# Kernel optimization log

Measured on AMD Instinct MI355X. Metric: run time of the kernel, lower is better.

The kernel has to match this reference:

```python
import jax, jax.numpy as jnp
import numpy as np

N, IN_DIM, OUT_DIM, HEADS = 3072, 512, 64, 8
EDGE_PROB = 0.01
NEG_SLOPE = 0.2


def setup_inputs() -> dict:
    key = jax.random.key(0)
    k1, k2, k3, k4, k5 = jax.random.split(key, 5)
    x = jax.random.normal(k1, (N, IN_DIM), dtype=jnp.float32)
    # sparse-ish dense adjacency mask with self-loops
    adj = (jax.random.uniform(k2, (N, N)) < EDGE_PROB).astype(jnp.float32)
    adj = jnp.maximum(adj, jnp.eye(N, dtype=jnp.float32))
    W = jax.random.normal(k3, (HEADS, IN_DIM, OUT_DIM), dtype=jnp.float32) * 0.1
    a_src = jax.random.normal(k4, (HEADS, OUT_DIM), dtype=jnp.float32) * 0.1
    a_dst = jax.random.normal(k5, (HEADS, OUT_DIM), dtype=jnp.float32) * 0.1
    return {"x": x, "adj": adj, "W": W, "a_src": a_src, "a_dst": a_dst}


def reference(x, adj, W, a_src, a_dst):
    # per-head linear projection: [H, N, OUT]
    h = jnp.einsum("ni,hio->hno", x, W)
    # attention logits e_ij = LeakyReLU(a_src . h_i + a_dst . h_j)
    f_src = jnp.einsum("hno,ho->hn", h, a_src)  # [H, N]
    f_dst = jnp.einsum("hno,ho->hn", h, a_dst)  # [H, N]
    e = f_src[:, :, None] + f_dst[:, None, :]   # [H, N, N]
    e = jax.nn.leaky_relu(e, negative_slope=NEG_SLOPE)
    # mask non-edges, row-softmax over neighbors
    e = jnp.where(adj[None] > 0, e, jnp.float32(-1e9))
    att = jax.nn.softmax(e, axis=-1)             # [H, N, N]
    # aggregate neighbor features per head
    out = jnp.einsum("hij,hjo->hio", att, h)     # [H, N, OUT]
    # concat heads along feature dim -> [N, H*OUT]
    return out.transpose(1, 0, 2).reshape(N, HEADS * OUT_DIM)
```

## Files before the change

kernel.cpp:

```cpp
#include <hip/hip_runtime.h>

#define N_NODES 3072
#define IN_DIM 512
#define OUT_DIM 64
#define HEADS 8
#define NEG_SLOPE 0.2f
#define MAX_E 128
#define KTILES (IN_DIM / 32)

typedef __attribute__((ext_vector_type(8))) short bf16x8;
typedef __attribute__((ext_vector_type(4))) float f32x4;

__device__ inline unsigned short f2bf(float f) {
    union { float f; unsigned u; } v; v.f = f;
    unsigned r = (v.u + 0x7FFF + ((v.u >> 16) & 1)) >> 16;
    return (unsigned short)r;
}

__global__ __launch_bounds__(256, 3) void gat_proj(
    const float* __restrict__ x, const float* __restrict__ W,
    const float* __restrict__ a_src, const float* __restrict__ a_dst,
    unsigned short* __restrict__ hb, float* __restrict__ fsrc,
    float* __restrict__ fdst) {
    __shared__ float hs[32][OUT_DIM + 1];

    const int t = threadIdx.x;
    const int lane = t & 63;
    const int w = t >> 6;
    const int head = blockIdx.y;
    const int m0 = blockIdx.x * 32;

    const int colr = lane & 15;
    const int kq = lane >> 4;

    const float* wp0 = W + ((size_t)head * IN_DIM + kq * 8) * OUT_DIM + w * 16 + colr;
    const float* xr0 = x + (size_t)(m0 + colr) * IN_DIM + kq * 8;
    const float* xr1 = xr0 + (size_t)16 * IN_DIM;

    f32x4 acc0 = {0.f, 0.f, 0.f, 0.f};
    f32x4 acc1 = {0.f, 0.f, 0.f, 0.f};
#pragma unroll
    for (int kt = 0; kt < KTILES; ++kt) {
        const float* wp = wp0 + (size_t)kt * 32 * OUT_DIM;
        bf16x8 bv;
#pragma unroll
        for (int j = 0; j < 8; ++j) bv[j] = (short)f2bf(wp[(size_t)j * OUT_DIM]);

        const float4* p0 = (const float4*)(xr0 + kt * 32);
        const float4* p1 = (const float4*)(xr1 + kt * 32);
        float4 u0 = p0[0], u1 = p0[1];
        float4 v0 = p1[0], v1 = p1[1];
        bf16x8 a0, a1;
        a0[0] = (short)f2bf(u0.x); a0[1] = (short)f2bf(u0.y);
        a0[2] = (short)f2bf(u0.z); a0[3] = (short)f2bf(u0.w);
        a0[4] = (short)f2bf(u1.x); a0[5] = (short)f2bf(u1.y);
        a0[6] = (short)f2bf(u1.z); a0[7] = (short)f2bf(u1.w);
        a1[0] = (short)f2bf(v0.x); a1[1] = (short)f2bf(v0.y);
        a1[2] = (short)f2bf(v0.z); a1[3] = (short)f2bf(v0.w);
        a1[4] = (short)f2bf(v1.x); a1[5] = (short)f2bf(v1.y);
        a1[6] = (short)f2bf(v1.z); a1[7] = (short)f2bf(v1.w);
        acc0 = __builtin_amdgcn_mfma_f32_16x16x32_bf16(a0, bv, acc0, 0, 0, 0);
        acc1 = __builtin_amdgcn_mfma_f32_16x16x32_bf16(a1, bv, acc1, 0, 0, 0);
    }

    const int col = w * 16 + colr;
    const int r0 = kq * 4;
    unsigned short* hp = hb + (size_t)m0 * (HEADS * OUT_DIM) + head * OUT_DIM + col;
#pragma unroll
    for (int i2 = 0; i2 < 4; ++i2) {
        hs[r0 + i2][col] = acc0[i2];
        hs[r0 + 16 + i2][col] = acc1[i2];
        hp[(size_t)(r0 + i2) * (HEADS * OUT_DIM)] = f2bf(acc0[i2]);
        hp[(size_t)(r0 + 16 + i2) * (HEADS * OUT_DIM)] = f2bf(acc1[i2]);
    }
    __syncthreads();

    {
        const float* av = (t < 128 ? a_src : a_dst) + head * OUT_DIM;
        const int tt = t & 127;
        const int row = tt >> 2, part = tt & 3;
        float s = 0.f;
#pragma unroll
        for (int n = 0; n < 16; ++n) s += hs[row][part * 16 + n] * av[part * 16 + n];
        s += __shfl_xor(s, 1, 64);
        s += __shfl_xor(s, 2, 64);
        if (part == 0) {
            float* dst = (t < 128 ? fsrc : fdst);
            dst[head * N_NODES + m0 + row] = s;
        }
    }
}

__global__ __launch_bounds__(256) void gat_agg(
    const float* __restrict__ adj, const unsigned short* __restrict__ hb,
    const float* __restrict__ fsrc, const float* __restrict__ fdst,
    float* __restrict__ out) {
    __shared__ int s_idx[MAX_E];
    __shared__ float s_p[HEADS][MAX_E];
    __shared__ int s_cnt;

    const int i = blockIdx.x;
    const int t = threadIdx.x;
    if (t == 0) s_cnt = 0;
    __syncthreads();

    const float4* arow4 = (const float4*)(adj + (size_t)i * N_NODES);
#pragma unroll
    for (int it = 0; it < 3; ++it) {
        const int jj = t + it * 256;
        float4 v = arow4[jj];
        const int j = jj * 4;
        if (v.x > 0.f) { int s = atomicAdd(&s_cnt, 1); if (s < MAX_E) s_idx[s] = j; }
        if (v.y > 0.f) { int s = atomicAdd(&s_cnt, 1); if (s < MAX_E) s_idx[s] = j + 1; }
        if (v.z > 0.f) { int s = atomicAdd(&s_cnt, 1); if (s < MAX_E) s_idx[s] = j + 2; }
        if (v.w > 0.f) { int s = atomicAdd(&s_cnt, 1); if (s < MAX_E) s_idx[s] = j + 3; }
    }
    __syncthreads();
    const int E = min(s_cnt, MAX_E);

    const int w = t >> 6;
    const int lane = t & 63;
    const int half = lane >> 5;
    const int sl = lane & 31;
    const int head = 2 * w + half;

    const float fi = fsrc[head * N_NODES + i];

    float m = -1e30f;
    for (int k = sl; k < E; k += 32) {
        float e = fi + fdst[head * N_NODES + s_idx[k]];
        e = e > 0.f ? e : NEG_SLOPE * e;
        s_p[head][k] = e;
        m = fmaxf(m, e);
    }
#pragma unroll
    for (int o = 16; o; o >>= 1) m = fmaxf(m, __shfl_xor(m, o, 64));

    float sum = 0.f;
    for (int k = sl; k < E; k += 32) {
        float p = __expf(s_p[head][k] - m);
        s_p[head][k] = p;
        sum += p;
    }
#pragma unroll
    for (int o = 16; o; o >>= 1) sum += __shfl_xor(sum, o, 64);
    const float inv = 1.f / sum;

    __syncthreads();

    const unsigned short* hbase = hb + head * OUT_DIM + sl * 2;
    float a0 = 0.f, a1 = 0.f;
#pragma unroll 8
    for (int k = 0; k < E; ++k) {
        const int j = s_idx[k];
        const float p = s_p[head][k];
        const unsigned u = *(const unsigned*)(hbase + (size_t)j * (HEADS * OUT_DIM));
        a0 = fmaf(p, __uint_as_float(u << 16), a0);
        a1 = fmaf(p, __uint_as_float(u & 0xffff0000u), a1);
    }
    float2 r = {a0 * inv, a1 * inv};
    *(float2*)(out + (size_t)i * (HEADS * OUT_DIM) + head * OUT_DIM + sl * 2) = r;
}

extern "C" void kernel_launch(void* const* d_in, const int* in_sizes, int n_in,
                              void* d_out, int out_size, void* d_ws, size_t ws_size,
                              hipStream_t stream) {
    const float* x     = (const float*)d_in[0];
    const float* adj   = (const float*)d_in[1];
    const float* W     = (const float*)d_in[2];
    const float* a_src = (const float*)d_in[3];
    const float* a_dst = (const float*)d_in[4];
    float* out = (float*)d_out;

    float* fsrc = (float*)d_ws;
    float* fdst = fsrc + HEADS * N_NODES;
    unsigned short* hb = (unsigned short*)(fdst + HEADS * N_NODES);

    gat_proj<<<dim3(N_NODES / 32, HEADS), 256, 0, stream>>>(
        x, W, a_src, a_dst, hb, fsrc, fdst);
    gat_agg<<<N_NODES, 256, 0, stream>>>(adj, hb, fsrc, fdst, out);
}
```

Baseline: 124.1 us.

## Move adjacency scan into projection kernel and stage x tile in LDS

Appends adjacency-row scan blocks to the projection launch so the memory-bound adj scan runs alongside the projection MFMA work. The scan writes neighbor indices and counts to workspace, and the aggregation kernel then only reads the compacted list. The projection now converts the x tile to bf16 once into swizzled shared memory instead of reading it per k-tile from global. The cost is extra workspace traffic for the index lists and a heterogeneous grid with 32KB shared memory per block.

New measurement: 107.3 us. 13.5% less time.

```diff
diff --git a/kernel.cpp b/kernel.cpp
--- a/kernel.cpp
+++ b/kernel.cpp
@@ -7,6 +7,7 @@
 #define NEG_SLOPE 0.2f
 #define MAX_E 128
 #define KTILES (IN_DIM / 32)
+#define PROJ_BLOCKS (N_NODES / 32 * HEADS)
 
 typedef __attribute__((ext_vector_type(8))) short bf16x8;
 typedef __attribute__((ext_vector_type(4))) float f32x4;
@@ -17,65 +18,79 @@
     return (unsigned short)r;
 }
 
-__global__ __launch_bounds__(256, 3) void gat_proj(
+__global__ __launch_bounds__(256) void gat_proj_scan(
     const float* __restrict__ x, const float* __restrict__ W,
+    const float* __restrict__ adj,
     const float* __restrict__ a_src, const float* __restrict__ a_dst,
     unsigned short* __restrict__ hb, float* __restrict__ fsrc,
-    float* __restrict__ fdst) {
-    __shared__ float hs[32][OUT_DIM + 1];
-
+    float* __restrict__ fdst, int* __restrict__ e_idx, int* __restrict__ e_cnt) {
+    __shared__ __align__(16) char smem[32768];
+
+    const int b = blockIdx.x;
     const int t = threadIdx.x;
-    const int lane = t & 63;
-    const int w = t >> 6;
-    const int head = blockIdx.y;
-    const int m0 = blockIdx.x * 32;
-
-    const int colr = lane & 15;
-    const int kq = lane >> 4;
-
-    const float* wp0 = W + ((size_t)head * IN_DIM + kq * 8) * OUT_DIM + w * 16 + colr;
-    const float* xr0 = x + (size_t)(m0 + colr) * IN_DIM + kq * 8;
-    const float* xr1 = xr0 + (size_t)16 * IN_DIM;
-
-    f32x4 acc0 = {0.f, 0.f, 0.f, 0.f};
-    f32x4 acc1 = {0.f, 0.f, 0.f, 0.f};
-#pragma unroll
-    for (int kt = 0; kt < KTILES; ++kt) {
-        const float* wp = wp0 + (size_t)kt * 32 * OUT_DIM;
-        bf16x8 bv;
-#pragma unroll
-        for (int j = 0; j < 8; ++j) bv[j] = (short)f2bf(wp[(size_t)j * OUT_DIM]);
-
-        const float4* p0 = (const float4*)(xr0 + kt * 32);
-        const float4* p1 = (const float4*)(xr1 + kt * 32);
-        float4 u0 = p0[0], u1 = p0[1];
-        float4 v0 = p1[0], v1 = p1[1];
-        bf16x8 a0, a1;
-        a0[0] = (short)f2bf(u0.x); a0[1] = (short)f2bf(u0.y);
-        a0[2] = (short)f2bf(u0.z); a0[3] = (short)f2bf(u0.w);
-        a0[4] = (short)f2bf(u1.x); a0[5] = (short)f2bf(u1.y);
-        a0[6] = (short)f2bf(u1.z); a0[7] = (short)f2bf(u1.w);
-        a1[0] = (short)f2bf(v0.x); a1[1] = (short)f2bf(v0.y);
-        a1[2] = (short)f2bf(v0.z); a1[3] = (short)f2bf(v0.w);
-        a1[4] = (short)f2bf(v1.x); a1[5] = (short)f2bf(v1.y);
-        a1[6] = (short)f2bf(v1.z); a1[7] = (short)f2bf(v1.w);
-        acc0 = __builtin_amdgcn_mfma_f32_16x16x32_bf16(a0, bv, acc0, 0, 0, 0);
-        acc1 = __builtin_amdgcn_mfma_f32_16x16x32_bf16(a1, bv, acc1, 0, 0, 0);
-    }
-
-    const int col = w * 16 + colr;
-    const int r0 = kq * 4;
-    unsigned short* hp = hb + (size_t)m0 * (HEADS * OUT_DIM) + head * OUT_DIM + col;
-#pragma unroll
-    for (int i2 = 0; i2 < 4; ++i2) {
-        hs[r0 + i2][col] = acc0[i2];
-        hs[r0 + 16 + i2][col] = acc1[i2];
-        hp[(size_t)(r0 + i2) * (HEADS * OUT_DIM)] = f2bf(acc0[i2]);
-        hp[(size_t)(r0 + 16 + i2) * (HEADS * OUT_DIM)] = f2bf(acc1[i2]);
-    }
-    __syncthreads();
-
-    {
+
+    if (b < PROJ_BLOCKS) {
+        short* xs = (short*)smem;
+        const int lane = t & 63;
+        const int w = t >> 6;
+        const int head = b / 96;
+        const int rtp = b % 96;
+        const int m0 = rtp * 32;
+
+        {
+            const int r = t >> 3, c8 = t & 7;
+            const float* xrow = x + (size_t)(m0 + r) * IN_DIM;
+#pragma unroll
+            for (int qq = 0; qq < 8; ++qq) {
+                const int k0 = c8 * 8 + qq * 64;
+                const float4* xp = (const float4*)(xrow + k0);
+                float4 v0 = xp[0], v1 = xp[1];
+                bf16x8 rv;
+                rv[0] = (short)f2bf(v0.x); rv[1] = (short)f2bf(v0.y);
+                rv[2] = (short)f2bf(v0.z); rv[3] = (short)f2bf(v0.w);
+                rv[4] = (short)f2bf(v1.x); rv[5] = (short)f2bf(v1.y);
+                rv[6] = (short)f2bf(v1.z); rv[7] = (short)f2bf(v1.w);
+                const int kt = (c8 >> 2) + qq * 2;
+                const int l16 = (r & 15) | ((c8 & 3) << 4);
+                const int idx16 = ((r >> 4) * 16 + kt) * 64 + (l16 ^ ((kt & 3) << 2));
+                ((bf16x8*)xs)[idx16] = rv;
+            }
+        }
+        __syncthreads();
+
+        const int colr = lane & 15;
+        const int kq = lane >> 4;
+        const float* wbase = W + ((size_t)head * IN_DIM + kq * 8) * OUT_DIM + w * 16 + colr;
+
+        f32x4 acc0 = {0.f, 0.f, 0.f, 0.f};
+        f32x4 acc1 = {0.f, 0.f, 0.f, 0.f};
+#pragma unroll
+        for (int kt = 0; kt < KTILES; ++kt) {
+            const float* wp = wbase + (size_t)kt * 32 * OUT_DIM;
+            bf16x8 bv;
+#pragma unroll
+            for (int j = 0; j < 8; ++j) bv[j] = (short)f2bf(wp[(size_t)j * OUT_DIM]);
+            const int sw = (kt & 3) << 2;
+            bf16x8 a0 = ((const bf16x8*)xs)[kt * 64 + (lane ^ sw)];
+            bf16x8 a1 = ((const bf16x8*)xs)[(16 + kt) * 64 + (lane ^ sw)];
+            acc0 = __builtin_amdgcn_mfma_f32_16x16x32_bf16(a0, bv, acc0, 0, 0, 0);
+            acc1 = __builtin_amdgcn_mfma_f32_16x16x32_bf16(a1, bv, acc1, 0, 0, 0);
+        }
+        __syncthreads();
+
+        float (*hs)[OUT_DIM + 1] = (float (*)[OUT_DIM + 1])smem;
+        const int col = w * 16 + colr;
+        const int r0 = kq * 4;
+        unsigned short* hp = hb + (size_t)m0 * (HEADS * OUT_DIM) + head * OUT_DIM + col;
+#pragma unroll
+        for (int i2 = 0; i2 < 4; ++i2) {
+            hs[r0 + i2][col] = acc0[i2];
+            hs[r0 + 16 + i2][col] = acc1[i2];
+            hp[(size_t)(r0 + i2) * (HEADS * OUT_DIM)] = f2bf(acc0[i2]);
+            hp[(size_t)(r0 + 16 + i2) * (HEADS * OUT_DIM)] = f2bf(acc1[i2]);
+        }
+        __syncthreads();
+
         const float* av = (t < 128 ? a_src : a_dst) + head * OUT_DIM;
         const int tt = t & 127;
         const int row = tt >> 2, part = tt & 3;
@@ -88,35 +103,44 @@
             float* dst = (t < 128 ? fsrc : fdst);
             dst[head * N_NODES + m0 + row] = s;
         }
+    } else {
+        int* s_idx = (int*)smem;
+        int* s_cnt = (int*)(smem + MAX_E * 4);
+        const int i = b - PROJ_BLOCKS;
+        if (t == 0) *s_cnt = 0;
+        __syncthreads();
+
+        const float4* arow4 = (const float4*)(adj + (size_t)i * N_NODES);
+#pragma unroll
+        for (int it = 0; it < 3; ++it) {
+            const int jj = t + it * 256;
+            float4 v = arow4[jj];
+            const int j = jj * 4;
+            if (v.x > 0.f) { int s = atomicAdd(s_cnt, 1); if (s < MAX_E) s_idx[s] = j; }
+            if (v.y > 0.f) { int s = atomicAdd(s_cnt, 1); if (s < MAX_E) s_idx[s] = j + 1; }
+            if (v.z > 0.f) { int s = atomicAdd(s_cnt, 1); if (s < MAX_E) s_idx[s] = j + 2; }
+            if (v.w > 0.f) { int s = atomicAdd(s_cnt, 1); if (s < MAX_E) s_idx[s] = j + 3; }
+        }
+        __syncthreads();
+        const int E = min(*s_cnt, MAX_E);
+        if (t < E) e_idx[(size_t)i * MAX_E + t] = s_idx[t];
+        if (t == 0) e_cnt[i] = E;
     }
 }
 
 __global__ __launch_bounds__(256) void gat_agg(
-    const float* __restrict__ adj, const unsigned short* __restrict__ hb,
+    const int* __restrict__ e_idx, const int* __restrict__ e_cnt,
+    const unsigned short* __restrict__ hb,
     const float* __restrict__ fsrc, const float* __restrict__ fdst,
     float* __restrict__ out) {
     __shared__ int s_idx[MAX_E];
     __shared__ float s_p[HEADS][MAX_E];
-    __shared__ int s_cnt;
 
     const int i = blockIdx.x;
     const int t = threadIdx.x;
-    if (t == 0) s_cnt = 0;
+    const int E = e_cnt[i];
+    if (t < E) s_idx[t] = e_idx[(size_t)i * MAX_E + t];
     __syncthreads();
-
-    const float4* arow4 = (const float4*)(adj + (size_t)i * N_NODES);
-#pragma unroll
-    for (int it = 0; it < 3; ++it) {
-        const int jj = t + it * 256;
-        float4 v = arow4[jj];
-        const int j = jj * 4;
-        if (v.x > 0.f) { int s = atomicAdd(&s_cnt, 1); if (s < MAX_E) s_idx[s] = j; }
-        if (v.y > 0.f) { int s = atomicAdd(&s_cnt, 1); if (s < MAX_E) s_idx[s] = j + 1; }
-        if (v.z > 0.f) { int s = atomicAdd(&s_cnt, 1); if (s < MAX_E) s_idx[s] = j + 2; }
-        if (v.w > 0.f) { int s = atomicAdd(&s_cnt, 1); if (s < MAX_E) s_idx[s] = j + 3; }
-    }
-    __syncthreads();
-    const int E = min(s_cnt, MAX_E);
 
     const int w = t >> 6;
     const int lane = t & 63;
@@ -175,8 +199,10 @@
     float* fsrc = (float*)d_ws;
     float* fdst = fsrc + HEADS * N_NODES;
     unsigned short* hb = (unsigned short*)(fdst + HEADS * N_NODES);
-
-    gat_proj<<<dim3(N_NODES / 32, HEADS), 256, 0, stream>>>(
-        x, W, a_src, a_dst, hb, fsrc, fdst);
-    gat_agg<<<N_NODES, 256, 0, stream>>>(adj, hb, fsrc, fdst, out);
-}
+    int* e_idx = (int*)(hb + (size_t)N_NODES * HEADS * OUT_DIM);
+    int* e_cnt = e_idx + (size_t)N_NODES * MAX_E;
+
+    gat_proj_scan<<<PROJ_BLOCKS + N_NODES, 256, 0, stream>>>(
+        x, W, adj, a_src, a_dst, hb, fsrc, fdst, e_idx, e_cnt);
+    gat_agg<<<N_NODES, 256, 0, stream>>>(e_idx, e_cnt, hb, fsrc, fdst, out);
+}
```
